# Kernel optimization log

Hardware: AMD Instinct MI355X
Metric: run time of the kernel (lower is better)

Reference implementation:

```python
import jax, jax.numpy as jnp
import numpy as np

MU, SIGMA = -9.1232, 3.5412
FFT_SIZES = [8, 16, 32, 64]
HOP_SIZES = [2, 4, 8, 16]
EPS_MAG, EPS_SC = 1e-7, 1e-8


def hann_periodic(n):
    # torch.hann_window default (periodic=True)
    return 0.5 * (1.0 - jnp.cos(2.0 * jnp.pi * jnp.arange(n, dtype=jnp.float32) / n))


def stft_mag(xf, n_fft, hop):
    # xf: (rows, T). Matches torch.stft(center=True, pad_mode='reflect', onesided).
    pad = n_fft // 2
    xp = jnp.pad(xf, ((0, 0), (pad, pad)), mode='reflect')
    n_frames = 1 + (xp.shape[-1] - n_fft) // hop
    idx = jnp.arange(n_frames)[:, None] * hop + jnp.arange(n_fft)[None, :]
    frames = xp[:, idx] * hann_periodic(n_fft)  # (rows, n_frames, n_fft)
    spec = jnp.fft.rfft(frames, axis=-1)        # (rows, n_frames, n_fft//2+1)
    return jnp.abs(spec) + EPS_MAG


def setup_inputs() -> dict:
    key = jax.random.key(0)
    k1, k2 = jax.random.split(key)
    x = jax.random.normal(k1, (32, 1, 128, 1024), dtype=jnp.float32)
    y = jax.random.normal(k2, (32, 1, 128, 1024), dtype=jnp.float32)
    return {"x": x, "y": y}


def reference(x, y):
    B, C, F_mel, T = x.shape
    x_flat = jnp.exp(x * SIGMA + MU).reshape(-1, T)  # un-normalize log-mel -> linear
    y_flat = jnp.exp(y * SIGMA + MU).reshape(-1, T)
    loss_sc = jnp.float32(0.0)
    loss_mag = jnp.float32(0.0)
    for n_fft, hop in zip(FFT_SIZES, HOP_SIZES):
        x_mag = stft_mag(x_flat, n_fft, hop)
        y_mag = stft_mag(y_flat, n_fft, hop)
        sc = jnp.linalg.norm((y_mag - x_mag).ravel()) / (
            jnp.linalg.norm(y_mag.ravel()) + EPS_SC)
        mag = jnp.mean(jnp.abs(jnp.log(x_mag) - jnp.log(y_mag)))
        loss_sc = loss_sc + sc
        loss_mag = loss_mag + mag
    n = len(FFT_SIZES)
    return (loss_sc / n, loss_mag / n)
```

## Files before the change

### kernel.cpp

```cpp
#include <hip/hip_runtime.h>
#include <math.h>

static constexpr float kSigma = 3.5412f;
static constexpr float kMu    = -9.1232f;

constexpr double kPId = 3.14159265358979323846264338327950288;

constexpr double tp_sin(double r) {
    const double r2 = r * r;
    double t = r, s = r;
    t *= -r2 / (2.0 * 3.0);   s += t;
    t *= -r2 / (4.0 * 5.0);   s += t;
    t *= -r2 / (6.0 * 7.0);   s += t;
    t *= -r2 / (8.0 * 9.0);   s += t;
    t *= -r2 / (10.0 * 11.0); s += t;
    t *= -r2 / (12.0 * 13.0); s += t;
    return s;
}
constexpr double tp_cos(double r) {
    const double r2 = r * r;
    double t = 1.0, c = 1.0;
    t *= -r2 / (1.0 * 2.0);   c += t;
    t *= -r2 / (3.0 * 4.0);   c += t;
    t *= -r2 / (5.0 * 6.0);   c += t;
    t *= -r2 / (7.0 * 8.0);   c += t;
    t *= -r2 / (9.0 * 10.0);  c += t;
    t *= -r2 / (11.0 * 12.0); c += t;
    return c;
}
constexpr float ctw_c(int k, int n) {
    const int kk = ((k % n) + n) % n;
    const int q = (4 * kk) / n;
    const int num = 4 * kk - q * n;
    const double r = (2.0 * kPId * num) / (4.0 * n);
    const double cr = tp_cos(r), sr = tp_sin(r);
    return (float)(q == 0 ? cr : q == 1 ? -sr : q == 2 ? -cr : sr);
}
constexpr float ctw_ns(int k, int n) {
    const int kk = ((k % n) + n) % n;
    const int q = (4 * kk) / n;
    const int num = 4 * kk - q * n;
    const double r = (2.0 * kPId * num) / (4.0 * n);
    const double cr = tp_cos(r), sr = tp_sin(r);
    const double s = (q == 0 ? sr : q == 1 ? cr : q == 2 ? -sr : -cr);
    return (float)(-s);
}

__device__ __forceinline__ float pair_swap(float v) {
    return __int_as_float(__builtin_amdgcn_mov_dpp(__float_as_int(v), 0xB1, 0xF, 0xF, true));
}

#define DECLZ \
    float zr0=0.f,zi0=0.f, zr1=0.f,zi1=0.f, zr2=0.f,zi2=0.f, zr3=0.f,zi3=0.f, \
          zr4=0.f,zi4=0.f, zr5=0.f,zi5=0.f, zr6=0.f,zi6=0.f, zr7=0.f,zi7=0.f, \
          zr8=0.f,zi8=0.f, zr9=0.f,zi9=0.f, zr10=0.f,zi10=0.f, zr11=0.f,zi11=0.f; \
    (void)zr0;(void)zi0;(void)zr11;(void)zi11;

#define UPDB(n, m) \
    if constexpr ((n) >= 1 && (n) <= NB) { \
        constexpr int   k_ = (BSTART + (n) - 1) * ((m) + TAU * HH); \
        constexpr float c_ = ctw_c(k_, NN); \
        constexpr float s_ = ctw_ns(k_, NN); \
        zr##n = fmaf(d, c_, zr##n);  zi##n = fmaf(d, s_, zi##n); \
    }

#define ALLB(m) UPDB(1,m) UPDB(2,m) UPDB(3,m) UPDB(4,m) UPDB(5,m) \
                UPDB(6,m) UPDB(7,m) UPDB(8,m) UPDB(9,m) UPDB(10,m)

#define UPD_M(m) \
    if constexpr ((m) < HH) { \
        const float d = ps[off + TAU*HH + NN + (m)] - ps[off + TAU*HH + (m)]; \
        ALLB(m) \
        if constexpr (((m) & 7) == 7) __builtin_amdgcn_sched_barrier(0); \
    }
#define WRM_M(m) \
    if constexpr ((m) < HH) { \
        const float d = ps[TAU*HH + (m)]; \
        ALLB(m) \
        if constexpr (((m) & 7) == 7) __builtin_amdgcn_sched_barrier(0); \
    }

#define FORM(M) M(0) M(1) M(2) M(3) M(4) M(5) M(6) M(7) \
                M(8) M(9) M(10) M(11) M(12) M(13) M(14) M(15)

#define EMTB(nm, nc, np) \
    if constexpr (((nc) - 1) >= EJ0 && ((nc) - 1) < EJ0 + EN) { \
        constexpr int BG = BSTART + (nc) - 1; \
        float wr, wi; \
        if constexpr (BG == 0) { \
            const float s_ = (PH==0) ? zr##np : (PH==1) ? -zi##np : (PH==2) ? -zr##np : zi##np; \
            wr = 0.5f*zr##nc - 0.5f*s_;  wi = 0.5f*zi##nc; \
        } else if constexpr (BG == NN/2) { \
            const float s_ = (PH==0) ? zr##nm : (PH==1) ? zi##nm : (PH==2) ? -zr##nm : -zi##nm; \
            wr = 0.5f*zr##nc - 0.5f*s_;  wi = 0.5f*zi##nc; \
        } else { \
            const float tr = (PH==0) ? (zr##nm + zr##np) : (PH==1) ? (zi##nm - zi##np) \
                           : (PH==2) ? (-zr##nm - zr##np) : (zi##np - zi##nm); \
            const float ti = (PH==0) ? (zi##nm + zi##np) : (PH==1) ? (zr##np - zr##nm) \
                           : (PH==2) ? (-zi##nm - zi##np) : (zr##nm - zr##np); \
            wr = fmaf(-0.25f, tr, 0.5f*zr##nc);  wi = fmaf(-0.25f, ti, 0.5f*zi##nc); \
        } \
        const float pm   = fmaf(wr, wr, wi*wi); \
        const float mag  = sqrtf(pm) + 1e-7f; \
        const float lg   = __log2f(mag); \
        const float mago = pair_swap(mag); \
        const float lgo  = pair_swap(lg); \
        const float d_   = mag - mago; \
        sd2 = fmaf(d_, d_, sd2); \
        sy2 = fmaf(mag, mag, sy2); \
        slg += fabsf(lg - lgo); \
    }

#define FOREMT(M) M(0,1,2) M(1,2,3) M(2,3,4) M(3,4,5) M(4,5,6) \
                  M(5,6,7) M(6,7,8) M(7,8,9) M(8,9,10) M(9,10,11)

#define SLOT(t) { constexpr int TAU = (t); constexpr int PH = (t); FOREMT(EMTB) FORM(UPD_M) }
#define WARM(t) { constexpr int TAU = (t); FORM(WRM_M) }

template <int NN, int BSTART, int NB, int EJ0, int EN, int OFF>
__device__ __forceinline__ void run_group(const float* __restrict__ ps_,
                                          int seg, int sig,
                                          float& sd2, float& sy2, float& slg)
{
    constexpr int HH = NN / 4;
    constexpr int FF = 4096 / NN + 1;
    constexpr int NQ = FF >> 5;
    const int t0 = (seg * FF) >> 3;
    const int t1 = ((seg + 1) * FF) >> 3;
    const int L  = t1 - t0;
    const float* __restrict__ ps = ps_ + OFF + t0 * HH;

    DECLZ
    WARM(0) WARM(1) WARM(2) WARM(3)

    int off = 0;
#pragma unroll
    for (int q = 0; q < NQ; ++q) {
        SLOT(0) SLOT(1) SLOT(2) SLOT(3)
        off += 4 * HH;
    }
    if (L > 4 * NQ) { SLOT(0) }
}

__global__ __launch_bounds__(1024, 4)
void fused_sdft_kernel(const float* __restrict__ xg, const float* __restrict__ yg,
                       float* __restrict__ acc)
{
    constexpr int RS = 1106;
    __shared__ float ldsx[8][RS];
    __shared__ float ldsy[8][RS];
    __shared__ float red[16][3];

    const int tid  = threadIdx.x;
    const int row0 = blockIdx.x << 3;

#pragma unroll 1
    for (int task = tid; task < 4096; task += 1024) {
        const int q = task & 255, rr = (task >> 8) & 7, sg = task >> 11;
        const float* __restrict__ src = sg ? yg : xg;
        const float4 v = reinterpret_cast<const float4*>(src)[((row0 + rr) << 8) + q];
        float* dst = (sg ? &ldsy[rr][0] : &ldsx[rr][0]) + 32 + (q << 2);
        dst[0] = __expf(fmaf(v.x, kSigma, kMu));
        dst[1] = __expf(fmaf(v.y, kSigma, kMu));
        dst[2] = __expf(fmaf(v.z, kSigma, kMu));
        dst[3] = __expf(fmaf(v.w, kSigma, kMu));
    }
#pragma unroll 1
    for (int task = tid; task < 1280; task += 1024) {
        const int p = task % 80, rem_ = task / 80;
        const int rr = rem_ & 7, sg = rem_ >> 3;
        const int j = (p < 32) ? p : (1024 + p);
        float v = 0.f;
        if (j < 1088) {
            const int i = (j < 32) ? (32 - j) : (2078 - j);
            const float* __restrict__ src = sg ? yg : xg;
            v = __expf(fmaf(src[((row0 + rr) << 10) + i], kSigma, kMu));
        }
        (sg ? ldsy[rr] : ldsx[rr])[j] = v;
    }
    __syncthreads();

    const int wid  = tid >> 6, lane = tid & 63;
    const int idx  = ((wid & 1) << 6) | lane;
    const int seg  = idx >> 4;
    const int row  = (idx >> 1) & 7;
    const int sig  = idx & 1;
    const float* ps = sig ? &ldsy[row][0] : &ldsx[row][0];

    float sd2 = 0.f, sy2 = 0.f, slg = 0.f;
    switch (wid >> 1) {
        case 0:  run_group<64,  0,  9, 0, 8,  0>(ps, seg, sig, sd2, sy2, slg); break;
        case 1:  run_group<64,  7, 10, 1, 8,  0>(ps, seg, sig, sd2, sy2, slg); break;
        case 2:  run_group<64, 15, 10, 1, 8,  0>(ps, seg, sig, sd2, sy2, slg); break;
        case 3:  run_group<64, 23, 10, 1, 9,  0>(ps, seg, sig, sd2, sy2, slg); break;
        case 4:  run_group<32,  0,  9, 0, 8, 16>(ps, seg, sig, sd2, sy2, slg); break;
        case 5:  run_group<32,  7, 10, 1, 9, 16>(ps, seg, sig, sd2, sy2, slg); break;
        case 6:  run_group<16,  0,  9, 0, 9, 24>(ps, seg, sig, sd2, sy2, slg); break;
        default: run_group< 8,  0,  5, 0, 5, 28>(ps, seg, sig, sd2, sy2, slg); break;
    }

    if (!sig) sy2 = 0.f;
#pragma unroll
    for (int o = 32; o > 0; o >>= 1) {
        sd2 += __shfl_down(sd2, o);
        sy2 += __shfl_down(sy2, o);
        slg += __shfl_down(slg, o);
    }
    if (lane == 0) { red[wid][0] = sd2; red[wid][1] = sy2; red[wid][2] = slg; }
    __syncthreads();
    if (tid < 16) {
        const int w2 = tid >> 1;
        const int res = (w2 < 4) ? 3 : (w2 < 6) ? 2 : (w2 == 6) ? 1 : 0;
        atomicAdd(&acc[(res * 3 + 0) * 64], red[tid][0]);
        atomicAdd(&acc[(res * 3 + 1) * 64], red[tid][1]);
        atomicAdd(&acc[(res * 3 + 2) * 64], red[tid][2]);
    }
}

__global__ void finalize_kernel(const float* __restrict__ acc, float* __restrict__ out)
{
    if (threadIdx.x == 0 && blockIdx.x == 0) {
        const float nel[4] = {10506240.f, 9474048.f, 8982528.f, 8785920.f};
        float sc = 0.f, mg = 0.f;
#pragma unroll
        for (int r = 0; r < 4; ++r) {
            const float a0 = acc[(r * 3 + 0) * 64];
            const float a1 = acc[(r * 3 + 1) * 64];
            const float a2 = acc[(r * 3 + 2) * 64];
            sc += sqrtf(a0 * 0.5f) / (sqrtf(a1) + 1e-8f);
            mg += a2 * 0.34657359028f / nel[r];
        }
        out[0] = sc * 0.25f;
        out[1] = mg * 0.25f;
    }
}

extern "C" void kernel_launch(void* const* d_in, const int* in_sizes, int n_in,
                              void* d_out, int out_size, void* d_ws, size_t ws_size,
                              hipStream_t stream)
{
    const float* x = (const float*)d_in[0];
    const float* y = (const float*)d_in[1];
    float* out = (float*)d_out;
    float* acc = (float*)d_ws;

    hipMemsetAsync(acc, 0, 12 * 64 * sizeof(float), stream);
    fused_sdft_kernel<<<512, 1024, 0, stream>>>(x, y, acc);
    finalize_kernel<<<1, 64, 0, stream>>>(acc, out);
}
```

Before: 165.7 us.

## Split fused STFT kernel into per-resolution launches with 256-thread blocks

Replaces the single fused kernel, where 1024-thread blocks each handled 8 rows across all four FFT sizes, with four launches, one per FFT size, using 256-thread blocks on 4 rows each. Wave-to-segment mapping is now set by template parameters, and each block does a single atomic per accumulator. The aim is to remove load imbalance between resolutions and to allow smaller, more flexible blocks. In exchange, every launch reloads and re-exponentiates the inputs, so global reads and expf work are quadrupled, and there are extra launch overheads.

```diff
diff --git a/kernel.cpp b/kernel.cpp
--- a/kernel.cpp
+++ b/kernel.cpp
@@ -117,16 +117,15 @@
 #define SLOT(t) { constexpr int TAU = (t); constexpr int PH = (t); FOREMT(EMTB) FORM(UPD_M) }
 #define WARM(t) { constexpr int TAU = (t); FORM(WRM_M) }
 
-template <int NN, int BSTART, int NB, int EJ0, int EN, int OFF>
+template <int NN, int BSTART, int NB, int EJ0, int EN, int OFF, int LOG2SEGS>
 __device__ __forceinline__ void run_group(const float* __restrict__ ps_,
-                                          int seg, int sig,
-                                          float& sd2, float& sy2, float& slg)
+                                          int seg, float& sd2, float& sy2, float& slg)
 {
     constexpr int HH = NN / 4;
     constexpr int FF = 4096 / NN + 1;
-    constexpr int NQ = FF >> 5;
-    const int t0 = (seg * FF) >> 3;
-    const int t1 = ((seg + 1) * FF) >> 3;
+    constexpr int NQ = FF >> (LOG2SEGS + 2);
+    const int t0 = (seg * FF) >> LOG2SEGS;
+    const int t1 = ((seg + 1) * FF) >> LOG2SEGS;
     const int L  = t1 - t0;
     const float* __restrict__ ps = ps_ + OFF + t0 * HH;
 
@@ -142,21 +141,22 @@
     if (L > 4 * NQ) { SLOT(0) }
 }
 
-__global__ __launch_bounds__(1024, 4)
-void fused_sdft_kernel(const float* __restrict__ xg, const float* __restrict__ yg,
-                       float* __restrict__ acc)
+template <int NN, int NGROUPS>
+__global__ __launch_bounds__(256, 4)
+void sdft_kernel(const float* __restrict__ xg, const float* __restrict__ yg,
+                 float* __restrict__ acc )
 {
     constexpr int RS = 1106;
-    __shared__ float ldsx[8][RS];
-    __shared__ float ldsy[8][RS];
-    __shared__ float red[16][3];
+    __shared__ float ldsx[4][RS];
+    __shared__ float ldsy[4][RS];
+    __shared__ float red[4][3];
 
     const int tid  = threadIdx.x;
-    const int row0 = blockIdx.x << 3;
+    const int row0 = blockIdx.x << 2;
 
 #pragma unroll 1
-    for (int task = tid; task < 4096; task += 1024) {
-        const int q = task & 255, rr = (task >> 8) & 7, sg = task >> 11;
+    for (int task = tid; task < 2048; task += 256) {
+        const int q = task & 255, rr = (task >> 8) & 3, sg = task >> 10;
         const float* __restrict__ src = sg ? yg : xg;
         const float4 v = reinterpret_cast<const float4*>(src)[((row0 + rr) << 8) + q];
         float* dst = (sg ? &ldsy[rr][0] : &ldsx[rr][0]) + 32 + (q << 2);
@@ -166,9 +166,9 @@
         dst[3] = __expf(fmaf(v.w, kSigma, kMu));
     }
 #pragma unroll 1
-    for (int task = tid; task < 1280; task += 1024) {
+    for (int task = tid; task < 640; task += 256) {
         const int p = task % 80, rem_ = task / 80;
-        const int rr = rem_ & 7, sg = rem_ >> 3;
+        const int rr = rem_ & 3, sg = rem_ >> 2;
         const int j = (p < 32) ? p : (1024 + p);
         float v = 0.f;
         if (j < 1088) {
@@ -180,23 +180,31 @@
     }
     __syncthreads();
 
+    constexpr int GL2 = (NGROUPS == 4) ? 2 : (NGROUPS == 2) ? 1 : 0;
+    constexpr int LOG2SEGS = 5 - GL2;
     const int wid  = tid >> 6, lane = tid & 63;
-    const int idx  = ((wid & 1) << 6) | lane;
-    const int seg  = idx >> 4;
-    const int row  = (idx >> 1) & 7;
-    const int sig  = idx & 1;
+    const int group  = wid & (NGROUPS - 1);
+    const int segblk = wid >> GL2;
+    const int seg  = (segblk << 3) | (lane >> 3);
+    const int row  = (lane >> 1) & 3;
+    const int sig  = lane & 1;
     const float* ps = sig ? &ldsy[row][0] : &ldsx[row][0];
 
     float sd2 = 0.f, sy2 = 0.f, slg = 0.f;
-    switch (wid >> 1) {
-        case 0:  run_group<64,  0,  9, 0, 8,  0>(ps, seg, sig, sd2, sy2, slg); break;
-        case 1:  run_group<64,  7, 10, 1, 8,  0>(ps, seg, sig, sd2, sy2, slg); break;
-        case 2:  run_group<64, 15, 10, 1, 8,  0>(ps, seg, sig, sd2, sy2, slg); break;
-        case 3:  run_group<64, 23, 10, 1, 9,  0>(ps, seg, sig, sd2, sy2, slg); break;
-        case 4:  run_group<32,  0,  9, 0, 8, 16>(ps, seg, sig, sd2, sy2, slg); break;
-        case 5:  run_group<32,  7, 10, 1, 9, 16>(ps, seg, sig, sd2, sy2, slg); break;
-        case 6:  run_group<16,  0,  9, 0, 9, 24>(ps, seg, sig, sd2, sy2, slg); break;
-        default: run_group< 8,  0,  5, 0, 5, 28>(ps, seg, sig, sd2, sy2, slg); break;
+    if constexpr (NN == 64) {
+        switch (group) {
+            case 0:  run_group<64,  0,  9, 0, 8,  0, LOG2SEGS>(ps, seg, sd2, sy2, slg); break;
+            case 1:  run_group<64,  7, 10, 1, 8,  0, LOG2SEGS>(ps, seg, sd2, sy2, slg); break;
+            case 2:  run_group<64, 15, 10, 1, 8,  0, LOG2SEGS>(ps, seg, sd2, sy2, slg); break;
+            default: run_group<64, 23, 10, 1, 9,  0, LOG2SEGS>(ps, seg, sd2, sy2, slg); break;
+        }
+    } else if constexpr (NN == 32) {
+        if (group == 0) run_group<32,  0,  9, 0, 8, 16, LOG2SEGS>(ps, seg, sd2, sy2, slg);
+        else            run_group<32,  7, 10, 1, 9, 16, LOG2SEGS>(ps, seg, sd2, sy2, slg);
+    } else if constexpr (NN == 16) {
+        run_group<16, 0, 9, 0, 9, 24, LOG2SEGS>(ps, seg, sd2, sy2, slg);
+    } else {
+        run_group< 8, 0, 5, 0, 5, 28, LOG2SEGS>(ps, seg, sd2, sy2, slg);
     }
 
     if (!sig) sy2 = 0.f;
@@ -208,12 +216,10 @@
     }
     if (lane == 0) { red[wid][0] = sd2; red[wid][1] = sy2; red[wid][2] = slg; }
     __syncthreads();
-    if (tid < 16) {
-        const int w2 = tid >> 1;
-        const int res = (w2 < 4) ? 3 : (w2 < 6) ? 2 : (w2 == 6) ? 1 : 0;
-        atomicAdd(&acc[(res * 3 + 0) * 64], red[tid][0]);
-        atomicAdd(&acc[(res * 3 + 1) * 64], red[tid][1]);
-        atomicAdd(&acc[(res * 3 + 2) * 64], red[tid][2]);
+    if (tid == 0) {
+        atomicAdd(&acc[0],   red[0][0] + red[1][0] + red[2][0] + red[3][0]);
+        atomicAdd(&acc[64],  red[0][1] + red[1][1] + red[2][1] + red[3][1]);
+        atomicAdd(&acc[128], red[0][2] + red[1][2] + red[2][2] + red[3][2]);
     }
 }
 
@@ -245,6 +251,11 @@
     float* acc = (float*)d_ws;
 
     hipMemsetAsync(acc, 0, 12 * 64 * sizeof(float), stream);
-    fused_sdft_kernel<<<512, 1024, 0, stream>>>(x, y, acc);
+
+    sdft_kernel<64, 4><<<1024, 256, 0, stream>>>(x, y, acc + 3 * 192);
+    sdft_kernel<32, 2><<<1024, 256, 0, stream>>>(x, y, acc + 2 * 192);
+    sdft_kernel<16, 1><<<1024, 256, 0, stream>>>(x, y, acc + 1 * 192);
+    sdft_kernel< 8, 1><<<1024, 256, 0, stream>>>(x, y, acc + 0 * 192);
+
     finalize_kernel<<<1, 64, 0, stream>>>(acc, out);
 }
```

New measurement: 144.2 us. 13.0% less time.
